# Performance work log

Hardware: AMD Instinct MI355X
Metric: run time of the kernel (lower is better)

The kernel has to match this reference:

```python
import jax, jax.numpy as jnp
import numpy as np

GROUP = 32          # microscale group size for both acts and weights
FP8_MAX = 448.0     # float8_e4m3fn max
FP4_TABLE = jnp.array([0.0, 0.5, 1.0, 1.5, 2.0, 3.0, 4.0, 6.0,
                       -0.0, -0.5, -1.0, -1.5, -2.0, -3.0, -4.0, -6.0], dtype=jnp.float32)


def _ue8m0_to_float(sf):
    # uint8 exponent byte placed directly into the fp32 exponent field: 2^(e-127)
    return jax.lax.bitcast_convert_type(sf.astype(jnp.uint32) << 23, jnp.float32)


def _dequant_mxfp4(w_packed, sf):
    # w_packed: [..., K//2] ints in [0,256), two e2m1 nibbles per byte (low nibble = even elem)
    lo = FP4_TABLE[w_packed & 0xF]
    hi = FP4_TABLE[(w_packed >> 4) & 0xF]
    w = jnp.stack([lo, hi], axis=-1).reshape(*w_packed.shape[:-1], -1)   # [..., K]
    s = _ue8m0_to_float(sf)                                              # [..., K//32]
    w = w.reshape(*sf.shape, GROUP) * s[..., None]
    return w.reshape(*w_packed.shape[:-1], 2 * w_packed.shape[-1])


def _quant_dequant_fp8(x):
    # Faithful to _deepseek_v4_stage_mega_moe_inputs_kernel: per-32-group amax,
    # scale = amax/448 rounded UP to a power of two (UE8M0), cast to fp8 e4m3.
    T, D = x.shape
    xg = x.reshape(T, D // GROUP, GROUP)
    amax = jnp.maximum(jnp.max(jnp.abs(xg), axis=-1), 1e-4)
    scale = amax / FP8_MAX
    bits = jax.lax.bitcast_convert_type(scale, jnp.uint32)
    exp = ((bits >> 23) & 0xFF) + ((bits & 0x7FFFFF) != 0).astype(jnp.uint32)
    exp = jnp.clip(exp, 1, 254)
    rscale = jax.lax.bitcast_convert_type(exp << 23, jnp.float32)
    q = (xg * (1.0 / rscale)[..., None]).astype(jnp.float8_e4m3fn)
    return (q.astype(jnp.float32) * rscale[..., None]).reshape(T, D)


def setup_inputs() -> dict:
    key = jax.random.key(0)
    ks = jax.random.split(key, 7)
    T, D, I, E, K = 512, 2048, 768, 16, 8
    hidden_states = jax.random.normal(ks[0], (T, D), dtype=jnp.float32)
    topk_weights = jax.random.uniform(ks[1], (T, K), dtype=jnp.float32)
    topk_weights = topk_weights / jnp.sum(topk_weights, axis=-1, keepdims=True)
    topk_ids = jax.random.randint(ks[2], (T, K), 0, E, dtype=jnp.int32)
    w13_weight = jax.random.randint(ks[3], (E, 2 * I, D // 2), 0, 256, dtype=jnp.int32)
    w13_weight_scale = jax.random.randint(ks[4], (E, 2 * I, D // GROUP), 120, 128, dtype=jnp.int32)
    w2_weight = jax.random.randint(ks[5], (E, D, I // 2), 0, 256, dtype=jnp.int32)
    w2_weight_scale = jax.random.randint(ks[6], (E, D, I // GROUP), 120, 128, dtype=jnp.int32)
    return {"hidden_states": hidden_states, "topk_weights": topk_weights,
            "topk_ids": topk_ids, "w13_weight": w13_weight,
            "w13_weight_scale": w13_weight_scale, "w2_weight": w2_weight,
            "w2_weight_scale": w2_weight_scale}


def reference(hidden_states, topk_weights, topk_ids, w13_weight, w13_weight_scale,
              w2_weight, w2_weight_scale):
    E = w13_weight.shape[0]
    I = w13_weight.shape[1] // 2
    x = _quant_dequant_fp8(hidden_states)                 # [T, D] fp8-quantized acts
    w13 = _dequant_mxfp4(w13_weight, w13_weight_scale)    # [E, 2I, D]
    w2 = _dequant_mxfp4(w2_weight, w2_weight_scale)       # [E, D, I]
    onehot = (topk_ids[:, :, None] == jnp.arange(E)[None, None, :]).astype(jnp.float32)  # [T,K,E]
    routed = jnp.any(onehot > 0, axis=1)                  # [T, E]
    Xe = routed.T[:, :, None].astype(x.dtype) * x[None]   # [E, T, D]
    h = jnp.einsum('etd,efd->etf', Xe, w13)               # [E, T, 2I]
    gate, up = h[..., :I], h[..., I:]
    a = jax.nn.silu(gate) * up                            # SiluAndMul
    ye = jnp.einsum('eti,edi->etd', a, w2)                # [E, T, D]
    comb = jnp.einsum('tke,tk->te', onehot, topk_weights) # [T, E] routing weights
    return jnp.einsum('te,etd->td', comb, ye)             # [T, D]
```

## Files before the change

### kernel.cpp

```cpp
#include <hip/hip_runtime.h>
#include <stdint.h>
#include <math.h>

#define T_TOK 512
#define DDIM  2048
#define IDIM  768
#define NEXP  16
#define TOPK  8
#define LDB   72
#define YW    1024

typedef __attribute__((ext_vector_type(8))) short bf16x8;
typedef __attribute__((ext_vector_type(4))) float f32x4;

__device__ __forceinline__ float e4m3_rtne(float f) {
  uint32_t u = __float_as_uint(f);
  uint32_t sign = u & 0x80000000u;
  uint32_t a = u & 0x7FFFFFFFu;
  float fa = __uint_as_float(a);
  float out;
  if (fa >= 0.015625f) {
    uint32_t lsb = (a >> 20) & 1u;
    a += 0x0007FFFFu + lsb;
    a &= 0xFFF00000u;
    out = __uint_as_float(a);
  } else {
    out = rintf(fa * 512.0f) * 0.001953125f;
  }
  return __uint_as_float(__float_as_uint(out) | sign);
}

__global__ __launch_bounds__(512) void qdq_route_kernel(
    const float* __restrict__ x, ushort* __restrict__ xq,
    const int* __restrict__ ids, const float* __restrict__ wts,
    int* __restrict__ counts, int* __restrict__ offsets,
    short* __restrict__ lists, float* __restrict__ combs,
    ushort* __restrict__ tpp, int* __restrict__ tpn)
{
  if ((int)blockIdx.x < (int)gridDim.x - 1) {
    int idx4 = blockIdx.x * 512 + threadIdx.x;
    float4 v = ((const float4*)x)[idx4];
    float a = fmaxf(fmaxf(fabsf(v.x), fabsf(v.y)), fmaxf(fabsf(v.z), fabsf(v.w)));
#pragma unroll
    for (int m = 4; m >= 1; m >>= 1)
      a = fmaxf(a, __shfl_xor(a, m, 8));
    a = fmaxf(a, 1e-4f);
    float scale = a / 448.0f;
    uint32_t b = __float_as_uint(scale);
    uint32_t ex = ((b >> 23) & 255u) + ((b & 0x7FFFFFu) ? 1u : 0u);
    ex = ex < 1u ? 1u : (ex > 254u ? 254u : ex);
    float rscale = __uint_as_float(ex << 23);
    float inv = 1.0f / rscale;
    uint32_t r0 = __float_as_uint(e4m3_rtne(v.x * inv) * rscale) >> 16;
    uint32_t r1 = __float_as_uint(e4m3_rtne(v.y * inv) * rscale) >> 16;
    uint32_t r2 = __float_as_uint(e4m3_rtne(v.z * inv) * rscale) >> 16;
    uint32_t r3 = __float_as_uint(e4m3_rtne(v.w * inv) * rscale) >> 16;
    ((uint2*)xq)[idx4] = make_uint2(r0 | (r1 << 16), r2 | (r3 << 16));
  } else {
    __shared__ int scnt[NEXP];
    int t = threadIdx.x;
    if (t < NEXP) scnt[t] = 0;
    __syncthreads();
    int  myid[TOPK];
    float myw[TOPK];
#pragma unroll
    for (int k = 0; k < TOPK; k++) { myid[k] = ids[t*TOPK+k]; myw[k] = wts[t*TOPK+k]; }
    int np = 0;
    for (int e = 0; e < NEXP; e++) {
      float s = 0.f; bool r = false;
#pragma unroll
      for (int k = 0; k < TOPK; k++) if (myid[k] == e) { s += myw[k]; r = true; }
      if (r) {
        int slot = atomicAdd(&scnt[e], 1);
        lists[(e<<9) + slot] = (short)t;
        combs[(e<<9) + slot] = s;
        tpp[t*TOPK + np] = (ushort)((e << 12) | slot);
        np++;
      }
    }
    tpn[t] = np;
    __syncthreads();
    if (t == 0) {
      int acc = 0;
      for (int e = 0; e < NEXP; e++) {
        offsets[e] = acc;
        int c = scnt[e];
        counts[e] = c;
        acc += c;
      }
      offsets[NEXP] = acc;
    }
  }
}

__device__ __forceinline__ uint32_t dec2(uint32_t w8, uint32_t S) {
  uint32_t lo = w8 & 15u, hi = (w8 >> 4) & 15u;
  uint32_t mlo = lo & 7u, mhi = hi & 7u;
  uint32_t clo = (mlo < 2u) ? 0u : mlo;
  uint32_t chi = (mhi < 2u) ? 0u : mhi;
  uint32_t blo = (mlo == 0u) ? 0u : ((S + clo) << 6);
  uint32_t bhi = (mhi == 0u) ? 0u : ((S + chi) << 6);
  blo |= (lo & 8u) << 12;
  bhi |= (hi & 8u) << 12;
  return blo | (bhi << 16);
}

__global__ __launch_bounds__(256,3) void gemm1_kernel(
    const ushort* __restrict__ xq, const int* __restrict__ w13,
    const int* __restrict__ w13s, const int* __restrict__ counts,
    const int* __restrict__ offsets, const short* __restrict__ lists,
    const float* __restrict__ combs, ushort* __restrict__ a_buf)
{
  const int e  = blockIdx.x;
  const int i0 = blockIdx.y << 5;
  const int m0 = blockIdx.z << 7;
  const int cnt = counts[e];
  if (m0 >= cnt) return;

  __shared__ __align__(16) ushort Bsh[2][64*LDB];
  __shared__ int   toks[128];
  __shared__ float cmbs[128];

  const int tid = threadIdx.x;
  if (tid < 128) {
    int m = m0 + tid; bool v = m < cnt;
    toks[tid] = v ? (int)lists[(e<<9)+m] : 0;
    cmbs[tid] = v ? combs[(e<<9)+m] : 0.f;
  }
  __syncthreads();

  const int wv = tid >> 6, l = tid & 63, l16 = l & 15, q = l >> 4;

  const ushort* arow[2];
#pragma unroll
  for (int i = 0; i < 2; i++)
    arow[i] = xq + (size_t)toks[wv*32 + i*16 + l16]*DDIM + q*8;

  const int rb = tid >> 2, hq = tid & 3;
  const int feat = (rb < 32) ? (i0 + rb) : (IDIM + i0 + (rb - 32));
  const int* wrow = w13 + ((size_t)e*(2*IDIM) + feat)*(DDIM/2) + hq*8;
  const int* srow = w13s + ((size_t)e*(2*IDIM) + feat)*(DDIM/32) + (hq >> 1);
  const int bdst = rb*LDB + hq*16;

  f32x4 acc[2][4];
#pragma unroll
  for (int i = 0; i < 2; i++)
#pragma unroll
    for (int j = 0; j < 4; j++) acc[i][j] = (f32x4){0.f,0.f,0.f,0.f};

  bf16x8 afr[2][2];
#pragma unroll
  for (int i = 0; i < 2; i++)
#pragma unroll
    for (int s = 0; s < 2; s++)
      afr[i][s] = *(const bf16x8*)(arow[i] + s*32);
  {
    int4 w0 = *(const int4*)(wrow);
    int4 w1 = *(const int4*)(wrow + 4);
    uint32_t S = (((uint32_t)srow[0]) - 1u) << 1;
    int wi[8] = {w0.x,w0.y,w0.z,w0.w, w1.x,w1.y,w1.z,w1.w};
    uint32_t od[8];
#pragma unroll
    for (int c = 0; c < 8; c++) od[c] = dec2((uint32_t)wi[c], S);
    ushort* d = &Bsh[0][bdst];
    *(uint4*)d       = make_uint4(od[0], od[1], od[2], od[3]);
    *(uint4*)(d + 8) = make_uint4(od[4], od[5], od[6], od[7]);
  }
  __syncthreads();

  for (int k0 = 0; k0 < DDIM; k0 += 64) {
    const int cur = (k0 >> 6) & 1;
    const bool more = (k0 + 64) < DDIM;

    int4 nw0, nw1; uint32_t nS = 0;
    bf16x8 nafr[2][2];
    if (more) {
      const int* wp = wrow + ((k0 + 64) >> 1);
      nw0 = *(const int4*)wp;
      nw1 = *(const int4*)(wp + 4);
      nS = (((uint32_t)srow[(k0 + 64) >> 5]) - 1u) << 1;
#pragma unroll
      for (int i = 0; i < 2; i++)
#pragma unroll
        for (int s = 0; s < 2; s++)
          nafr[i][s] = *(const bf16x8*)(arow[i] + k0 + 64 + s*32);
    }

#pragma unroll
    for (int s = 0; s < 2; s++) {
      bf16x8 bfr[4];
#pragma unroll
      for (int j = 0; j < 4; j++)
        bfr[j] = *(const bf16x8*)&Bsh[cur][(j*16 + l16)*LDB + s*32 + q*8];
#pragma unroll
      for (int i = 0; i < 2; i++)
#pragma unroll
        for (int j = 0; j < 4; j++)
          acc[i][j] = __builtin_amdgcn_mfma_f32_16x16x32_bf16(afr[i][s], bfr[j], acc[i][j], 0, 0, 0);
    }

    if (more) {
      int wi[8] = {nw0.x,nw0.y,nw0.z,nw0.w, nw1.x,nw1.y,nw1.z,nw1.w};
      uint32_t od[8];
#pragma unroll
      for (int c = 0; c < 8; c++) od[c] = dec2((uint32_t)wi[c], nS);
      ushort* d = &Bsh[1 - cur][bdst];
      *(uint4*)d       = make_uint4(od[0], od[1], od[2], od[3]);
      *(uint4*)(d + 8) = make_uint4(od[4], od[5], od[6], od[7]);
#pragma unroll
      for (int i = 0; i < 2; i++)
#pragma unroll
        for (int s = 0; s < 2; s++)
          afr[i][s] = nafr[i][s];
    }
    __syncthreads();
  }

  const int obase = offsets[e];
#pragma unroll
  for (int i = 0; i < 2; i++) {
#pragma unroll
    for (int r = 0; r < 4; r++) {
      int mrow = wv*32 + i*16 + q*4 + r;
      int gm = m0 + mrow;
      if (gm < cnt) {
        float c = cmbs[mrow];
        ushort* dst = a_buf + (size_t)(obase + gm)*IDIM + i0 + l16;
#pragma unroll
        for (int jj = 0; jj < 2; jj++) {
          float g = acc[i][jj][r], u = acc[i][jj+2][r];
          float val = (g / (1.f + expf(-g))) * u * c;
          uint32_t bb = __float_as_uint(val);
          bb += 0x7FFFu + ((bb >> 16) & 1u);
          dst[jj*16] = (ushort)(bb >> 16);
        }
      }
    }
  }
}

__global__ __launch_bounds__(256,3) void gemm2_kernel(
    const ushort* __restrict__ a_buf, const int* __restrict__ w2,
    const int* __restrict__ w2s, const int* __restrict__ counts,
    const int* __restrict__ offsets, ushort* __restrict__ ye, int yb)
{
  const int e  = blockIdx.x;
  const int n0 = yb + (blockIdx.y << 6);
  const int m0 = blockIdx.z << 7;
  const int cnt = counts[e];
  if (m0 >= cnt) return;

  __shared__ __align__(16) ushort Bsh[2][64*LDB];

  const int tid = threadIdx.x;
  const int wv = tid >> 6, l = tid & 63, l16 = l & 15, q = l >> 4;
  const int obase = offsets[e];

  const ushort* arow[2];
#pragma unroll
  for (int i = 0; i < 2; i++) {
    int gm = m0 + wv*32 + i*16 + l16;
    int rowc = (gm < cnt) ? gm : 0;
    arow[i] = a_buf + (size_t)(obase + rowc)*IDIM + q*8;
  }

  const int rb = tid >> 2, hq = tid & 3;
  const int* wrow = w2 + ((size_t)e*DDIM + n0 + rb)*(IDIM/2) + hq*8;
  const int* srow = w2s + ((size_t)e*DDIM + n0 + rb)*(IDIM/32) + (hq >> 1);
  const int bdst = rb*LDB + hq*16;

  f32x4 acc[2][4];
#pragma unroll
  for (int i = 0; i < 2; i++)
#pragma unroll
    for (int j = 0; j < 4; j++) acc[i][j] = (f32x4){0.f,0.f,0.f,0.f};

  bf16x8 afr[2][2];
#pragma unroll
  for (int i = 0; i < 2; i++)
#pragma unroll
    for (int s = 0; s < 2; s++)
      afr[i][s] = *(const bf16x8*)(arow[i] + s*32);
  {
    int4 w0 = *(const int4*)(wrow);
    int4 w1 = *(const int4*)(wrow + 4);
    uint32_t S = (((uint32_t)srow[0]) - 1u) << 1;
    int wi[8] = {w0.x,w0.y,w0.z,w0.w, w1.x,w1.y,w1.z,w1.w};
    uint32_t od[8];
#pragma unroll
    for (int c = 0; c < 8; c++) od[c] = dec2((uint32_t)wi[c], S);
    ushort* d = &Bsh[0][bdst];
    *(uint4*)d       = make_uint4(od[0], od[1], od[2], od[3]);
    *(uint4*)(d + 8) = make_uint4(od[4], od[5], od[6], od[7]);
  }
  __syncthreads();

  for (int k0 = 0; k0 < IDIM; k0 += 64) {
    const int cur = (k0 >> 6) & 1;
    const bool more = (k0 + 64) < IDIM;

    int4 nw0, nw1; uint32_t nS = 0;
    bf16x8 nafr[2][2];
    if (more) {
      const int* wp = wrow + ((k0 + 64) >> 1);
      nw0 = *(const int4*)wp;
      nw1 = *(const int4*)(wp + 4);
      nS = (((uint32_t)srow[(k0 + 64) >> 5]) - 1u) << 1;
#pragma unroll
      for (int i = 0; i < 2; i++)
#pragma unroll
        for (int s = 0; s < 2; s++)
          nafr[i][s] = *(const bf16x8*)(arow[i] + k0 + 64 + s*32);
    }

#pragma unroll
    for (int s = 0; s < 2; s++) {
      bf16x8 bfr[4];
#pragma unroll
      for (int j = 0; j < 4; j++)
        bfr[j] = *(const bf16x8*)&Bsh[cur][(j*16 + l16)*LDB + s*32 + q*8];
#pragma unroll
      for (int i = 0; i < 2; i++)
#pragma unroll
        for (int j = 0; j < 4; j++)
          acc[i][j] = __builtin_amdgcn_mfma_f32_16x16x32_bf16(afr[i][s], bfr[j], acc[i][j], 0, 0, 0);
    }

    if (more) {
      int wi[8] = {nw0.x,nw0.y,nw0.z,nw0.w, nw1.x,nw1.y,nw1.z,nw1.w};
      uint32_t od[8];
#pragma unroll
      for (int c = 0; c < 8; c++) od[c] = dec2((uint32_t)wi[c], nS);
      ushort* d = &Bsh[1 - cur][bdst];
      *(uint4*)d       = make_uint4(od[0], od[1], od[2], od[3]);
      *(uint4*)(d + 8) = make_uint4(od[4], od[5], od[6], od[7]);
#pragma unroll
      for (int i = 0; i < 2; i++)
#pragma unroll
        for (int s = 0; s < 2; s++)
          afr[i][s] = nafr[i][s];
    }
    __syncthreads();
  }

#pragma unroll
  for (int i = 0; i < 2; i++) {
#pragma unroll
    for (int r = 0; r < 4; r++) {
      int mrow = wv*32 + i*16 + q*4 + r;
      int gm = m0 + mrow;
      if (gm < cnt) {
        ushort* dst = ye + (size_t)(obase + gm)*YW + (n0 - yb) + l16;
#pragma unroll
        for (int j = 0; j < 4; j++) {
          uint32_t bb = __float_as_uint(acc[i][j][r]);
          bb += 0x7FFFu + ((bb >> 16) & 1u);
          dst[j*16] = (ushort)(bb >> 16);
        }
      }
    }
  }
}

__global__ void combine_kernel(const ushort* __restrict__ ye, const int* __restrict__ offsets,
                               const ushort* __restrict__ tpp, const int* __restrict__ tpn,
                               float* __restrict__ out, int yb) {
  int t = blockIdx.x;
  int np = tpn[t];
  int rows[TOPK];
#pragma unroll
  for (int j = 0; j < TOPK; j++) {
    if (j < np) {
      uint32_t v = tpp[t*TOPK + j];
      rows[j] = offsets[v >> 12] + (int)(v & 0xFFFu);
    } else rows[j] = -1;
  }
  for (int c = threadIdx.x; c < YW; c += 256) {
    float s = 0.f;
#pragma unroll
    for (int j = 0; j < TOPK; j++)
      if (rows[j] >= 0)
        s += __uint_as_float(((uint32_t)ye[(size_t)rows[j]*YW + c]) << 16);
    out[(size_t)t*DDIM + yb + c] = s;
  }
}

extern "C" void kernel_launch(void* const* d_in, const int* in_sizes, int n_in,
                              void* d_out, int out_size, void* d_ws, size_t ws_size,
                              hipStream_t stream)
{
  const float* x    = (const float*)d_in[0];
  const float* tw   = (const float*)d_in[1];
  const int*   tids = (const int*)d_in[2];
  const int*   w13  = (const int*)d_in[3];
  const int*   w13s = (const int*)d_in[4];
  const int*   w2   = (const int*)d_in[5];
  const int*   w2s  = (const int*)d_in[6];
  float* out = (float*)d_out;

  char* ws = (char*)d_ws;
  size_t off = 0;
  auto alloc = [&](size_t bytes) { void* p = ws + off; off = (off + bytes + 255) & ~(size_t)255; return p; };
  float* combs   = (float*)alloc((size_t)NEXP*T_TOK*4);
  short* lists   = (short*)alloc((size_t)NEXP*T_TOK*2);
  ushort* tpp    = (ushort*)alloc((size_t)T_TOK*TOPK*2);
  int*   tpn     = (int*)alloc((size_t)T_TOK*4);
  int*   counts  = (int*)alloc(64*4);
  int*   offsets = (int*)alloc(64*4);
  ushort* a_buf  = (ushort*)alloc((size_t)T_TOK*TOPK*IDIM*2);
  ushort* ye     = (ushort*)alloc((size_t)T_TOK*TOPK*YW*2);
  ushort* xq     = ye;

  qdq_route_kernel<<<(T_TOK*DDIM)/2048 + 1, 512, 0, stream>>>(
      x, xq, tids, tw, counts, offsets, lists, combs, tpp, tpn);
  gemm1_kernel<<<dim3(NEXP, IDIM/32, 4), 256, 0, stream>>>(
      xq, w13, w13s, counts, offsets, lists, combs, a_buf);
  for (int p = 0; p < DDIM/YW; p++) {
    gemm2_kernel<<<dim3(NEXP, YW/64, 4), 256, 0, stream>>>(
        a_buf, w2, w2s, counts, offsets, ye, p*YW);
    combine_kernel<<<T_TOK, 256, 0, stream>>>(ye, offsets, tpp, tpn, out, p*YW);
  }
}
```

Before: 310.3 us.

## Deepen prefetch to two stages in expert GEMMs and use single-slice output when workspace allows

```diff
diff --git a/kernel.cpp b/kernel.cpp
--- a/kernel.cpp
+++ b/kernel.cpp
@@ -8,7 +8,6 @@
 #define NEXP  16
 #define TOPK  8
 #define LDB   72
-#define YW    1024
 
 typedef __attribute__((ext_vector_type(8))) short bf16x8;
 typedef __attribute__((ext_vector_type(4))) float f32x4;
@@ -105,6 +104,15 @@
   return blo | (bhi << 16);
 }
 
+__device__ __forceinline__ void deq8(int4 w0, int4 w1, uint32_t S, ushort* dst) {
+  int wi[8] = {w0.x,w0.y,w0.z,w0.w, w1.x,w1.y,w1.z,w1.w};
+  uint32_t od[8];
+#pragma unroll
+  for (int c = 0; c < 8; c++) od[c] = dec2((uint32_t)wi[c], S);
+  *(uint4*)dst       = make_uint4(od[0], od[1], od[2], od[3]);
+  *(uint4*)(dst + 8) = make_uint4(od[4], od[5], od[6], od[7]);
+}
+
 __global__ __launch_bounds__(256,3) void gemm1_kernel(
     const ushort* __restrict__ xq, const int* __restrict__ w13,
     const int* __restrict__ w13s, const int* __restrict__ counts,
@@ -116,6 +124,7 @@
   const int m0 = blockIdx.z << 7;
   const int cnt = counts[e];
   if (m0 >= cnt) return;
+  const int NIT = DDIM / 64;
 
   __shared__ __align__(16) ushort Bsh[2][64*LDB];
   __shared__ int   toks[128];
@@ -148,71 +157,76 @@
 #pragma unroll
     for (int j = 0; j < 4; j++) acc[i][j] = (f32x4){0.f,0.f,0.f,0.f};
 
-  bf16x8 afr[2][2];
+  bf16x8 aA[2][2], aB[2][2];
+  int4 wA0, wA1, wB0, wB1; uint32_t SA, SB;
+
+  {
+    int4 t0 = *(const int4*)(wrow);
+    int4 t1 = *(const int4*)(wrow + 4);
+    uint32_t S = (((uint32_t)srow[0]) - 1u) << 1;
+    deq8(t0, t1, S, &Bsh[0][bdst]);
+  }
 #pragma unroll
   for (int i = 0; i < 2; i++)
 #pragma unroll
     for (int s = 0; s < 2; s++)
-      afr[i][s] = *(const bf16x8*)(arow[i] + s*32);
-  {
-    int4 w0 = *(const int4*)(wrow);
-    int4 w1 = *(const int4*)(wrow + 4);
-    uint32_t S = (((uint32_t)srow[0]) - 1u) << 1;
-    int wi[8] = {w0.x,w0.y,w0.z,w0.w, w1.x,w1.y,w1.z,w1.w};
-    uint32_t od[8];
-#pragma unroll
-    for (int c = 0; c < 8; c++) od[c] = dec2((uint32_t)wi[c], S);
-    ushort* d = &Bsh[0][bdst];
-    *(uint4*)d       = make_uint4(od[0], od[1], od[2], od[3]);
-    *(uint4*)(d + 8) = make_uint4(od[4], od[5], od[6], od[7]);
-  }
+      aA[i][s] = *(const bf16x8*)(arow[i] + s*32);
+  wA0 = *(const int4*)(wrow + 32); wA1 = *(const int4*)(wrow + 36);
+  SA  = (((uint32_t)srow[2]) - 1u) << 1;
+#pragma unroll
+  for (int i = 0; i < 2; i++)
+#pragma unroll
+    for (int s = 0; s < 2; s++)
+      aB[i][s] = *(const bf16x8*)(arow[i] + 64 + s*32);
   __syncthreads();
 
-  for (int k0 = 0; k0 < DDIM; k0 += 64) {
-    const int cur = (k0 >> 6) & 1;
-    const bool more = (k0 + 64) < DDIM;
-
-    int4 nw0, nw1; uint32_t nS = 0;
-    bf16x8 nafr[2][2];
-    if (more) {
-      const int* wp = wrow + ((k0 + 64) >> 1);
-      nw0 = *(const int4*)wp;
-      nw1 = *(const int4*)(wp + 4);
-      nS = (((uint32_t)srow[(k0 + 64) >> 5]) - 1u) << 1;
-#pragma unroll
-      for (int i = 0; i < 2; i++)
-#pragma unroll
-        for (int s = 0; s < 2; s++)
-          nafr[i][s] = *(const bf16x8*)(arow[i] + k0 + 64 + s*32);
-    }
-
+  for (int t = 0; t < NIT; t += 2) {
+    int t2 = t + 2 < NIT ? t + 2 : NIT - 1;
+    wB0 = *(const int4*)(wrow + t2*32);
+    wB1 = *(const int4*)(wrow + t2*32 + 4);
+    SB  = (((uint32_t)srow[t2*2]) - 1u) << 1;
 #pragma unroll
     for (int s = 0; s < 2; s++) {
       bf16x8 bfr[4];
 #pragma unroll
       for (int j = 0; j < 4; j++)
-        bfr[j] = *(const bf16x8*)&Bsh[cur][(j*16 + l16)*LDB + s*32 + q*8];
+        bfr[j] = *(const bf16x8*)&Bsh[0][(j*16 + l16)*LDB + s*32 + q*8];
 #pragma unroll
       for (int i = 0; i < 2; i++)
 #pragma unroll
         for (int j = 0; j < 4; j++)
-          acc[i][j] = __builtin_amdgcn_mfma_f32_16x16x32_bf16(afr[i][s], bfr[j], acc[i][j], 0, 0, 0);
-    }
-
-    if (more) {
-      int wi[8] = {nw0.x,nw0.y,nw0.z,nw0.w, nw1.x,nw1.y,nw1.z,nw1.w};
-      uint32_t od[8];
-#pragma unroll
-      for (int c = 0; c < 8; c++) od[c] = dec2((uint32_t)wi[c], nS);
-      ushort* d = &Bsh[1 - cur][bdst];
-      *(uint4*)d       = make_uint4(od[0], od[1], od[2], od[3]);
-      *(uint4*)(d + 8) = make_uint4(od[4], od[5], od[6], od[7]);
+          acc[i][j] = __builtin_amdgcn_mfma_f32_16x16x32_bf16(aA[i][s], bfr[j], acc[i][j], 0, 0, 0);
+    }
+    deq8(wA0, wA1, SA, &Bsh[1][bdst]);
+#pragma unroll
+    for (int i = 0; i < 2; i++)
+#pragma unroll
+      for (int s = 0; s < 2; s++)
+        aA[i][s] = *(const bf16x8*)(arow[i] + t2*64 + s*32);
+    __syncthreads();
+
+    int t3 = t + 3 < NIT ? t + 3 : NIT - 1;
+    wA0 = *(const int4*)(wrow + t3*32);
+    wA1 = *(const int4*)(wrow + t3*32 + 4);
+    SA  = (((uint32_t)srow[t3*2]) - 1u) << 1;
+#pragma unroll
+    for (int s = 0; s < 2; s++) {
+      bf16x8 bfr[4];
+#pragma unroll
+      for (int j = 0; j < 4; j++)
+        bfr[j] = *(const bf16x8*)&Bsh[1][(j*16 + l16)*LDB + s*32 + q*8];
 #pragma unroll
       for (int i = 0; i < 2; i++)
 #pragma unroll
-        for (int s = 0; s < 2; s++)
-          afr[i][s] = nafr[i][s];
-    }
+        for (int j = 0; j < 4; j++)
+          acc[i][j] = __builtin_amdgcn_mfma_f32_16x16x32_bf16(aB[i][s], bfr[j], acc[i][j], 0, 0, 0);
+    }
+    deq8(wB0, wB1, SB, &Bsh[0][bdst]);
+#pragma unroll
+    for (int i = 0; i < 2; i++)
+#pragma unroll
+      for (int s = 0; s < 2; s++)
+        aB[i][s] = *(const bf16x8*)(arow[i] + t3*64 + s*32);
     __syncthreads();
   }
 
@@ -242,13 +256,14 @@
 __global__ __launch_bounds__(256,3) void gemm2_kernel(
     const ushort* __restrict__ a_buf, const int* __restrict__ w2,
     const int* __restrict__ w2s, const int* __restrict__ counts,
-    const int* __restrict__ offsets, ushort* __restrict__ ye, int yb)
+    const int* __restrict__ offsets, ushort* __restrict__ ye, int yb, int yw)
 {
   const int e  = blockIdx.x;
   const int n0 = yb + (blockIdx.y << 6);
   const int m0 = blockIdx.z << 7;
   const int cnt = counts[e];
   if (m0 >= cnt) return;
+  const int NIT = IDIM / 64;
 
   __shared__ __align__(16) ushort Bsh[2][64*LDB];
 
@@ -275,71 +290,76 @@
 #pragma unroll
     for (int j = 0; j < 4; j++) acc[i][j] = (f32x4){0.f,0.f,0.f,0.f};
 
-  bf16x8 afr[2][2];
+  bf16x8 aA[2][2], aB[2][2];
+  int4 wA0, wA1, wB0, wB1; uint32_t SA, SB;
+
+  {
+    int4 t0 = *(const int4*)(wrow);
+    int4 t1 = *(const int4*)(wrow + 4);
+    uint32_t S = (((uint32_t)srow[0]) - 1u) << 1;
+    deq8(t0, t1, S, &Bsh[0][bdst]);
+  }
 #pragma unroll
   for (int i = 0; i < 2; i++)
 #pragma unroll
     for (int s = 0; s < 2; s++)
-      afr[i][s] = *(const bf16x8*)(arow[i] + s*32);
-  {
-    int4 w0 = *(const int4*)(wrow);
-    int4 w1 = *(const int4*)(wrow + 4);
-    uint32_t S = (((uint32_t)srow[0]) - 1u) << 1;
-    int wi[8] = {w0.x,w0.y,w0.z,w0.w, w1.x,w1.y,w1.z,w1.w};
-    uint32_t od[8];
-#pragma unroll
-    for (int c = 0; c < 8; c++) od[c] = dec2((uint32_t)wi[c], S);
-    ushort* d = &Bsh[0][bdst];
-    *(uint4*)d       = make_uint4(od[0], od[1], od[2], od[3]);
-    *(uint4*)(d + 8) = make_uint4(od[4], od[5], od[6], od[7]);
-  }
+      aA[i][s] = *(const bf16x8*)(arow[i] + s*32);
+  wA0 = *(const int4*)(wrow + 32); wA1 = *(const int4*)(wrow + 36);
+  SA  = (((uint32_t)srow[2]) - 1u) << 1;
+#pragma unroll
+  for (int i = 0; i < 2; i++)
+#pragma unroll
+    for (int s = 0; s < 2; s++)
+      aB[i][s] = *(const bf16x8*)(arow[i] + 64 + s*32);
   __syncthreads();
 
-  for (int k0 = 0; k0 < IDIM; k0 += 64) {
-    const int cur = (k0 >> 6) & 1;
-    const bool more = (k0 + 64) < IDIM;
-
-    int4 nw0, nw1; uint32_t nS = 0;
-    bf16x8 nafr[2][2];
-    if (more) {
-      const int* wp = wrow + ((k0 + 64) >> 1);
-      nw0 = *(const int4*)wp;
-      nw1 = *(const int4*)(wp + 4);
-      nS = (((uint32_t)srow[(k0 + 64) >> 5]) - 1u) << 1;
-#pragma unroll
-      for (int i = 0; i < 2; i++)
-#pragma unroll
-        for (int s = 0; s < 2; s++)
-          nafr[i][s] = *(const bf16x8*)(arow[i] + k0 + 64 + s*32);
-    }
-
+  for (int t = 0; t < NIT; t += 2) {
+    int t2 = t + 2 < NIT ? t + 2 : NIT - 1;
+    wB0 = *(const int4*)(wrow + t2*32);
+    wB1 = *(const int4*)(wrow + t2*32 + 4);
+    SB  = (((uint32_t)srow[t2*2]) - 1u) << 1;
 #pragma unroll
     for (int s = 0; s < 2; s++) {
       bf16x8 bfr[4];
 #pragma unroll
       for (int j = 0; j < 4; j++)
-        bfr[j] = *(const bf16x8*)&Bsh[cur][(j*16 + l16)*LDB + s*32 + q*8];
+        bfr[j] = *(const bf16x8*)&Bsh[0][(j*16 + l16)*LDB + s*32 + q*8];
 #pragma unroll
       for (int i = 0; i < 2; i++)
 #pragma unroll
         for (int j = 0; j < 4; j++)
-          acc[i][j] = __builtin_amdgcn_mfma_f32_16x16x32_bf16(afr[i][s], bfr[j], acc[i][j], 0, 0, 0);
-    }
-
-    if (more) {
-      int wi[8] = {nw0.x,nw0.y,nw0.z,nw0.w, nw1.x,nw1.y,nw1.z,nw1.w};
-      uint32_t od[8];
-#pragma unroll
-      for (int c = 0; c < 8; c++) od[c] = dec2((uint32_t)wi[c], nS);
-      ushort* d = &Bsh[1 - cur][bdst];
-      *(uint4*)d       = make_uint4(od[0], od[1], od[2], od[3]);
-      *(uint4*)(d + 8) = make_uint4(od[4], od[5], od[6], od[7]);
+          acc[i][j] = __builtin_amdgcn_mfma_f32_16x16x32_bf16(aA[i][s], bfr[j], acc[i][j], 0, 0, 0);
+    }
+    deq8(wA0, wA1, SA, &Bsh[1][bdst]);
+#pragma unroll
+    for (int i = 0; i < 2; i++)
+#pragma unroll
+      for (int s = 0; s < 2; s++)
+        aA[i][s] = *(const bf16x8*)(arow[i] + t2*64 + s*32);
+    __syncthreads();
+
+    int t3 = t + 3 < NIT ? t + 3 : NIT - 1;
+    wA0 = *(const int4*)(wrow + t3*32);
+    wA1 = *(const int4*)(wrow + t3*32 + 4);
+    SA  = (((uint32_t)srow[t3*2]) - 1u) << 1;
+#pragma unroll
+    for (int s = 0; s < 2; s++) {
+      bf16x8 bfr[4];
+#pragma unroll
+      for (int j = 0; j < 4; j++)
+        bfr[j] = *(const bf16x8*)&Bsh[1][(j*16 + l16)*LDB + s*32 + q*8];
 #pragma unroll
       for (int i = 0; i < 2; i++)
 #pragma unroll
-        for (int s = 0; s < 2; s++)
-          afr[i][s] = nafr[i][s];
-    }
+        for (int j = 0; j < 4; j++)
+          acc[i][j] = __builtin_amdgcn_mfma_f32_16x16x32_bf16(aB[i][s], bfr[j], acc[i][j], 0, 0, 0);
+    }
+    deq8(wB0, wB1, SB, &Bsh[0][bdst]);
+#pragma unroll
+    for (int i = 0; i < 2; i++)
+#pragma unroll
+      for (int s = 0; s < 2; s++)
+        aB[i][s] = *(const bf16x8*)(arow[i] + t3*64 + s*32);
     __syncthreads();
   }
 
@@ -350,7 +370,7 @@
       int mrow = wv*32 + i*16 + q*4 + r;
       int gm = m0 + mrow;
       if (gm < cnt) {
-        ushort* dst = ye + (size_t)(obase + gm)*YW + (n0 - yb) + l16;
+        ushort* dst = ye + (size_t)(obase + gm)*yw + (n0 - yb) + l16;
 #pragma unroll
         for (int j = 0; j < 4; j++) {
           uint32_t bb = __float_as_uint(acc[i][j][r]);
@@ -364,7 +384,7 @@
 
 __global__ void combine_kernel(const ushort* __restrict__ ye, const int* __restrict__ offsets,
                                const ushort* __restrict__ tpp, const int* __restrict__ tpn,
-                               float* __restrict__ out, int yb) {
+                               float* __restrict__ out, int yb, int yw) {
   int t = blockIdx.x;
   int np = tpn[t];
   int rows[TOPK];
@@ -375,12 +395,12 @@
       rows[j] = offsets[v >> 12] + (int)(v & 0xFFFu);
     } else rows[j] = -1;
   }
-  for (int c = threadIdx.x; c < YW; c += 256) {
+  for (int c = threadIdx.x; c < yw; c += 256) {
     float s = 0.f;
 #pragma unroll
     for (int j = 0; j < TOPK; j++)
       if (rows[j] >= 0)
-        s += __uint_as_float(((uint32_t)ye[(size_t)rows[j]*YW + c]) << 16);
+        s += __uint_as_float(((uint32_t)ye[(size_t)rows[j]*yw + c]) << 16);
     out[(size_t)t*DDIM + yb + c] = s;
   }
 }
@@ -408,16 +428,20 @@
   int*   counts  = (int*)alloc(64*4);
   int*   offsets = (int*)alloc(64*4);
   ushort* a_buf  = (ushort*)alloc((size_t)T_TOK*TOPK*IDIM*2);
-  ushort* ye     = (ushort*)alloc((size_t)T_TOK*TOPK*YW*2);
+  ushort* ye     = (ushort*)(ws + off);
   ushort* xq     = ye;
+
+  size_t ye_full = (size_t)T_TOK*TOPK*DDIM*2;
+  int nslice = (ws_size >= off + ye_full) ? 1 : 2;
+  int yw = DDIM / nslice;
 
   qdq_route_kernel<<<(T_TOK*DDIM)/2048 + 1, 512, 0, stream>>>(
       x, xq, tids, tw, counts, offsets, lists, combs, tpp, tpn);
   gemm1_kernel<<<dim3(NEXP, IDIM/32, 4), 256, 0, stream>>>(
       xq, w13, w13s, counts, offsets, lists, combs, a_buf);
-  for (int p = 0; p < DDIM/YW; p++) {
-    gemm2_kernel<<<dim3(NEXP, YW/64, 4), 256, 0, stream>>>(
-        a_buf, w2, w2s, counts, offsets, ye, p*YW);
-    combine_kernel<<<T_TOK, 256, 0, stream>>>(ye, offsets, tpp, tpn, out, p*YW);
-  }
-}
+  for (int p = 0; p < nslice; p++) {
+    gemm2_kernel<<<dim3(NEXP, yw/64, 4), 256, 0, stream>>>(
+        a_buf, w2, w2s, counts, offsets, ye, p*yw, yw);
+    combine_kernel<<<T_TOK, 256, 0, stream>>>(ye, offsets, tpp, tpn, out, p*yw, yw);
+  }
+}
```

Result: faster. 303.6 us (-2.2%).
